# Performance work log

Hardware: AMD Instinct MI355X
Metric: run time of the kernel (lower is better)

Reference implementation:

```python
import jax, jax.numpy as jnp
import numpy as np

NEG_INF = float(np.finfo(np.float32).min)


def setup_inputs() -> dict:
    key = jax.random.key(0)
    k1, k2, k3 = jax.random.split(key, 3)
    n_context, d_model = 4096, 2048
    x = jax.random.normal(k1, (n_context, d_model), dtype=jnp.float32)
    # nn.Linear default init scale ~ 1/sqrt(fan_in); use small weights for numeric sanity
    W_qk = jax.random.normal(k2, (d_model, d_model), dtype=jnp.float32) / np.sqrt(d_model)
    W_ov = jax.random.normal(k3, (d_model, d_model), dtype=jnp.float32) / np.sqrt(d_model)
    return {"x": x, "W_qk": W_qk, "W_ov": W_ov}


def reference(x, W_qk, W_ov):
    # Faithful to: softmax(X @ W_qk.T @ X.T + causal_mask) @ X @ W_ov.T
    # (biases of the torch Linears are never used in forward)
    n = x.shape[0]
    q = x @ W_qk.T                      # [n, d]
    scores = q @ x.T                    # [n, n]  (no 1/sqrt(d) scaling, as in source)
    causal = jnp.tril(jnp.ones((n, n), dtype=bool))
    scores = jnp.where(causal, scores, NEG_INF)  # additive -inf mask equivalent
    attn = jax.nn.softmax(scores, axis=-1)       # [n, n]
    out = (attn @ x) @ W_ov.T                    # [n, d]
    return out
```

## Files before the change

### kernel.cpp

```cpp
#include <hip/hip_runtime.h>
#include <hip/hip_bf16.h>
#include <stdint.h>
#include <stddef.h>

typedef _Float16 f16;
typedef __attribute__((ext_vector_type(8))) _Float16 f16x8;
typedef __attribute__((ext_vector_type(4))) float    f32x4;

constexpr int BM = 128, BN = 128, BK = 64;

#define GLOAD_LDS16(gp, lp)                                        \
    __builtin_amdgcn_global_load_lds(                              \
        (const __attribute__((address_space(1))) unsigned int*)(gp),\
        (__attribute__((address_space(3))) unsigned int*)(lp), 16, 0, 0)


template <int EPI, bool CAUSAL>
__global__ __launch_bounds__(256) void gemm_a2(
    const f16* __restrict__ Ah, const f16* __restrict__ Al,
    const f16* __restrict__ B,
    float* __restrict__ Cf, f16* __restrict__ Co, f16* __restrict__ Clo,
    int M, int N, int K)
{
    const int bx = blockIdx.x;
    const int by = blockIdx.y;
    if (CAUSAL && bx > by) return;

    const int tid   = threadIdx.x;
    const int lane  = tid & 63;
    const int wave  = tid >> 6;
    const int wm    = wave >> 1;
    const int wn    = wave & 1;
    const int lrow  = lane & 15;
    const int lquad = lane >> 4;

    __shared__ f16 sAh[BM * BK];
    __shared__ f16 sAl[BM * BK];
    __shared__ f16 sB [BN * BK];

    const int row0 = by * BM;
    const int col0 = bx * BN;

    const int srow = tid >> 3;
    const int scol = (((tid & 7) ^ ((tid >> 3) & 7))) * 8;
    const int lbase = wave * 512;

    f32x4 acc[4][4];
    const f32x4 fzero = {0.f, 0.f, 0.f, 0.f};
    #pragma unroll
    for (int i = 0; i < 4; ++i)
        #pragma unroll
        for (int j = 0; j < 4; ++j) acc[i][j] = fzero;

    for (int k0 = 0; k0 < K; k0 += BK) {
        __syncthreads();
        #pragma unroll
        for (int r = 0; r < 4; ++r) {
            const int trow = srow + 32 * r;
            const size_t ga = (size_t)(row0 + trow) * K + k0 + scol;
            const size_t gb = (size_t)(col0 + trow) * K + k0 + scol;
            const int ldst = lbase + r * 2048;
            GLOAD_LDS16(&Ah[ga], &sAh[ldst]);
            GLOAD_LDS16(&Al[ga], &sAl[ldst]);
            GLOAD_LDS16(&B [gb], &sB [ldst]);
        }
        __syncthreads();

        #pragma unroll
        for (int kk = 0; kk < 2; ++kk) {
            const int grpA = ((kk * 4 + lquad) ^ (lrow & 7)) * 8;
            f16x8 ah[4], al[4], bv[4];
            #pragma unroll
            for (int mi = 0; mi < 4; ++mi) {
                const int off = (wm * 64 + mi * 16 + lrow) * BK + grpA;
                ah[mi] = *reinterpret_cast<const f16x8*>(&sAh[off]);
                al[mi] = *reinterpret_cast<const f16x8*>(&sAl[off]);
            }
            #pragma unroll
            for (int ni = 0; ni < 4; ++ni)
                bv[ni] = *reinterpret_cast<const f16x8*>(
                    &sB[(wn * 64 + ni * 16 + lrow) * BK + grpA]);

            #pragma unroll
            for (int mi = 0; mi < 4; ++mi)
                #pragma unroll
                for (int ni = 0; ni < 4; ++ni) {
                    acc[mi][ni] = __builtin_amdgcn_mfma_f32_16x16x32_f16(
                        ah[mi], bv[ni], acc[mi][ni], 0, 0, 0);
                    acc[mi][ni] = __builtin_amdgcn_mfma_f32_16x16x32_f16(
                        al[mi], bv[ni], acc[mi][ni], 0, 0, 0);
                }
        }
    }

    #pragma unroll
    for (int mi = 0; mi < 4; ++mi) {
        #pragma unroll
        for (int ni = 0; ni < 4; ++ni) {
            #pragma unroll
            for (int r = 0; r < 4; ++r) {
                const int row = row0 + wm * 64 + mi * 16 + lquad * 4 + r;
                const int col = col0 + wn * 64 + ni * 16 + lrow;
                const size_t idx = (size_t)row * N + col;
                const float v = acc[mi][ni][r];
                if (EPI == 0) {
                    Cf[idx] = v;
                } else {
                    const f16 h = (f16)v;
                    Co[idx]  = h;
                    Clo[idx] = (f16)(v - (float)h);
                }
            }
        }
    }
}

template <int EPI, bool KCAUSAL>
__global__ __launch_bounds__(256) void gemm_plain(
    const f16* __restrict__ A, const f16* __restrict__ B,
    float* __restrict__ Cf, f16* __restrict__ Co,
    int M, int N, int K)
{
    const int bx = blockIdx.x;
    const int by = KCAUSAL ? (gridDim.y - 1 - blockIdx.y) : blockIdx.y;

    const int tid   = threadIdx.x;
    const int lane  = tid & 63;
    const int wave  = tid >> 6;
    const int wm    = wave >> 1;
    const int wn    = wave & 1;
    const int lrow  = lane & 15;
    const int lquad = lane >> 4;

    __shared__ f16 sA[BM * BK];
    __shared__ f16 sB[BN * BK];

    const int row0 = by * BM;
    const int col0 = bx * BN;

    const int srow = tid >> 3;
    const int scol = (((tid & 7) ^ ((tid >> 3) & 7))) * 8;
    const int lbase = wave * 512;

    f32x4 acc[4][4];
    const f32x4 fzero = {0.f, 0.f, 0.f, 0.f};
    #pragma unroll
    for (int i = 0; i < 4; ++i)
        #pragma unroll
        for (int j = 0; j < 4; ++j) acc[i][j] = fzero;

    const int Keff = KCAUSAL ? (by + 1) * BM : K;

    for (int k0 = 0; k0 < Keff; k0 += BK) {
        __syncthreads();
        #pragma unroll
        for (int r = 0; r < 4; ++r) {
            const int trow = srow + 32 * r;
            GLOAD_LDS16(&A[(size_t)(row0 + trow) * K + k0 + scol], &sA[lbase + r * 2048]);
            GLOAD_LDS16(&B[(size_t)(col0 + trow) * K + k0 + scol], &sB[lbase + r * 2048]);
        }
        __syncthreads();

        #pragma unroll
        for (int kk = 0; kk < 2; ++kk) {
            const int grpA = ((kk * 4 + lquad) ^ (lrow & 7)) * 8;
            f16x8 av[4], bv[4];
            #pragma unroll
            for (int mi = 0; mi < 4; ++mi)
                av[mi] = *reinterpret_cast<const f16x8*>(
                    &sA[(wm * 64 + mi * 16 + lrow) * BK + grpA]);
            #pragma unroll
            for (int ni = 0; ni < 4; ++ni)
                bv[ni] = *reinterpret_cast<const f16x8*>(
                    &sB[(wn * 64 + ni * 16 + lrow) * BK + grpA]);

            #pragma unroll
            for (int mi = 0; mi < 4; ++mi)
                #pragma unroll
                for (int ni = 0; ni < 4; ++ni)
                    acc[mi][ni] = __builtin_amdgcn_mfma_f32_16x16x32_f16(
                        av[mi], bv[ni], acc[mi][ni], 0, 0, 0);
        }
    }

    #pragma unroll
    for (int mi = 0; mi < 4; ++mi) {
        #pragma unroll
        for (int ni = 0; ni < 4; ++ni) {
            #pragma unroll
            for (int r = 0; r < 4; ++r) {
                const int row = row0 + wm * 64 + mi * 16 + lquad * 4 + r;
                const int col = col0 + wn * 64 + ni * 16 + lrow;
                const size_t idx = (size_t)row * N + col;
                const float v = acc[mi][ni][r];
                if (EPI == 0) Cf[idx] = v;
                else          Co[idx] = (f16)v;
            }
        }
    }
}

__global__ __launch_bounds__(256) void split_f32_f16(
    const float* __restrict__ in, f16* __restrict__ hi, f16* __restrict__ lo,
    size_t nelem)
{
    const size_t i = ((size_t)blockIdx.x * 256 + threadIdx.x) * 4;
    if (i >= nelem) return;
    const float4 v = *reinterpret_cast<const float4*>(in + i);
    union { f16 h[4]; ushort4 u; } H, L;
    H.h[0] = (f16)v.x; H.h[1] = (f16)v.y; H.h[2] = (f16)v.z; H.h[3] = (f16)v.w;
    *reinterpret_cast<ushort4*>(hi + i) = H.u;
    if (lo) {
        L.h[0] = (f16)(v.x - (float)H.h[0]);
        L.h[1] = (f16)(v.y - (float)H.h[1]);
        L.h[2] = (f16)(v.z - (float)H.h[2]);
        L.h[3] = (f16)(v.w - (float)H.h[3]);
        *reinterpret_cast<ushort4*>(lo + i) = L.u;
    }
}

__global__ __launch_bounds__(256) void softmax_rows(
    const float* __restrict__ S, f16* __restrict__ P, int n)
{
    const int row = blockIdx.x;
    const int len = row + 1;
    const int padlen = ((row >> 7) + 1) << 7;
    const float* srow = S + (size_t)row * n;
    f16* prow = P + (size_t)row * n;
    const int tid = threadIdx.x;
    const int lane = tid & 63, wave = tid >> 6;
    __shared__ float redm[4], reds[4];

    float m = -3.0e38f, s = 0.f;
    for (int j = tid; j < len; j += 256) {
        const float v = srow[j];
        const float mn = fmaxf(m, v);
        s = s * __expf(m - mn) + __expf(v - mn);
        m = mn;
    }
    #pragma unroll
    for (int off = 32; off; off >>= 1) {
        const float mo = __shfl_xor(m, off, 64);
        const float so = __shfl_xor(s, off, 64);
        const float mn = fmaxf(m, mo);
        s = s * __expf(m - mn) + so * __expf(mo - mn);
        m = mn;
    }
    if (lane == 0) { redm[wave] = m; reds[wave] = s; }
    __syncthreads();
    float M = redm[0], Sm = reds[0];
    #pragma unroll
    for (int w = 1; w < 4; ++w) {
        const float mn = fmaxf(M, redm[w]);
        Sm = Sm * __expf(M - mn) + reds[w] * __expf(redm[w] - mn);
        M = mn;
    }
    const float inv = 1.0f / Sm;

    const f16 z = (f16)0.0f;
    for (int j = tid; j < padlen; j += 256)
        prow[j] = (j < len) ? (f16)(__expf(srow[j] - M) * inv) : z;
}

__global__ __launch_bounds__(256) void transpose_f32_f16(
    const float* __restrict__ in, f16* __restrict__ out, int rows, int cols)
{
    __shared__ float tile[32][33];
    const int bx = blockIdx.x;
    const int by = blockIdx.y;
    const int tx = threadIdx.x & 31;
    const int ty = threadIdx.x >> 5;
    #pragma unroll
    for (int r = 0; r < 4; ++r)
        tile[ty + 8 * r][tx] = in[(size_t)(by * 32 + ty + 8 * r) * cols + bx * 32 + tx];
    __syncthreads();
    #pragma unroll
    for (int r = 0; r < 4; ++r)
        out[(size_t)(bx * 32 + ty + 8 * r) * rows + by * 32 + tx] =
            (f16)tile[tx][ty + 8 * r];
}

extern "C" void kernel_launch(void* const* d_in, const int* in_sizes, int n_in,
                              void* d_out, int out_size, void* d_ws, size_t ws_size,
                              hipStream_t stream)
{
    const int n = 4096, d = 2048;
    const float* x   = (const float*)d_in[0];
    const float* Wqk = (const float*)d_in[1];
    const float* Wov = (const float*)d_in[2];
    float* out = (float*)d_out;

    char* ws = (char*)d_ws;
    const size_t MB = 1 << 20;
    f16*   xh   = (f16*)  (ws);
    f16*   xl   = (f16*)  (ws + 16 * MB);
    f16*   Wh   = (f16*)  (ws + 32 * MB);
    f16*   Wovh = (f16*)  (ws + 40 * MB);
    f16*   xTh  = (f16*)  (ws + 48 * MB);
    f16*   qh   = (f16*)  (ws + 64 * MB);
    f16*   ql   = (f16*)  (ws + 80 * MB);
    float* S    = (float*)(ws + 96 * MB);
    f16*   P    = (f16*)  (ws);
    f16*   o    = (f16*)  (ws + 64 * MB);

    const dim3 blk(256);

    split_f32_f16<<<dim3((n * d) / (256 * 4)), blk, 0, stream>>>(x,   xh, xl, (size_t)n * d);
    split_f32_f16<<<dim3((d * d) / (256 * 4)), blk, 0, stream>>>(Wqk, Wh, nullptr, (size_t)d * d);
    split_f32_f16<<<dim3((d * d) / (256 * 4)), blk, 0, stream>>>(Wov, Wovh, nullptr, (size_t)d * d);
    transpose_f32_f16<<<dim3(d / 32, n / 32), blk, 0, stream>>>(x, xTh, n, d);

    gemm_a2<1, false><<<dim3(d / BN, n / BM), blk, 0, stream>>>(
        xh, xl, Wh, nullptr, qh, ql, n, d, d);

    gemm_a2<0, true><<<dim3(n / BN, n / BM), blk, 0, stream>>>(
        qh, ql, xh, S, nullptr, nullptr, n, n, d);

    softmax_rows<<<dim3(n), blk, 0, stream>>>(S, P, n);

    gemm_plain<2, true><<<dim3(d / BN, n / BM), blk, 0, stream>>>(
        P, xTh, nullptr, o, n, d, n);

    gemm_plain<0, false><<<dim3(d / BN, n / BM), blk, 0, stream>>>(
        o, Wovh, out, nullptr, n, d, d);
}
```

Baseline: 446.2 us.

## Use 8-wave 128x256 GEMM kernels with multi-buffered LDS prefetch pipelines

Replaces the two split-precision GEMMs (Q projection and causal scores) with an 8-wave, 128x256-tile kernel that double-buffers LDS and issues the next tile's global-to-LDS loads between MFMA phases. Explicit waitcnt and barriers plus s_setprio keep MFMA issue prioritised. The final output projection moves to a new triple-buffered 8-wave kernel. The aim is to hide global load latency and raise MFMA utilisation. The causal skip becomes coarser (2*bx > by), so some fully masked work is computed, and the larger LDS footprint may limit occupancy.

```diff
diff --git a/kernel.cpp b/kernel.cpp
--- a/kernel.cpp
+++ b/kernel.cpp
@@ -14,9 +14,20 @@
         (const __attribute__((address_space(1))) unsigned int*)(gp),\
         (__attribute__((address_space(3))) unsigned int*)(lp), 16, 0, 0)
 
+#define MFMA_TILE(AV, BV)                                                     \
+    do {                                                                      \
+        __builtin_amdgcn_s_setprio(1);                                        \
+        _Pragma("unroll")                                                     \
+        for (int mi_ = 0; mi_ < 4; ++mi_)                                     \
+            _Pragma("unroll")                                                 \
+            for (int ni_ = 0; ni_ < 4; ++ni_)                                 \
+                acc[mi_][ni_] = __builtin_amdgcn_mfma_f32_16x16x32_f16(       \
+                    (AV)[mi_], (BV)[ni_], acc[mi_][ni_], 0, 0, 0);            \
+        __builtin_amdgcn_s_setprio(0);                                        \
+    } while (0)
 
 template <int EPI, bool CAUSAL>
-__global__ __launch_bounds__(256) void gemm_a2(
+__global__ __launch_bounds__(512, 2) void gemm8_a2(
     const f16* __restrict__ Ah, const f16* __restrict__ Al,
     const f16* __restrict__ B,
     float* __restrict__ Cf, f16* __restrict__ Co, f16* __restrict__ Clo,
@@ -24,74 +35,126 @@
 {
     const int bx = blockIdx.x;
     const int by = blockIdx.y;
-    if (CAUSAL && bx > by) return;
+    if (CAUSAL && 2 * bx > by) return;
 
     const int tid   = threadIdx.x;
     const int lane  = tid & 63;
     const int wave  = tid >> 6;
-    const int wm    = wave >> 1;
-    const int wn    = wave & 1;
+    const int wm    = wave >> 2;
+    const int wn    = wave & 3;
     const int lrow  = lane & 15;
     const int lquad = lane >> 4;
 
-    __shared__ f16 sAh[BM * BK];
-    __shared__ f16 sAl[BM * BK];
-    __shared__ f16 sB [BN * BK];
-
-    const int row0 = by * BM;
-    const int col0 = bx * BN;
+    __shared__ f16 lds[2][32768];
+
+    const int row0 = by * 128;
+    const int col0 = bx * 256;
 
     const int srow = tid >> 3;
-    const int scol = (((tid & 7) ^ ((tid >> 3) & 7))) * 8;
-    const int lbase = wave * 512;
+    const int scol = ((tid & 7) ^ (srow & 7)) * 8;
+    const int loff = wave * 512;
+
+    const int g0 = ((lquad)     ^ (lrow & 7)) * 8;
+    const int g1 = ((4 + lquad) ^ (lrow & 7)) * 8;
+
+    const int arow = (wm * 64 + lrow) * 64;
+    const int brow = (wn * 64 + lrow) * 64 + 16384;
+
+    const f16* gAh = Ah + (size_t)(row0 + srow) * K + scol;
+    const f16* gAl = Al + (size_t)(row0 + srow) * K + scol;
+    const f16* gB  = B  + (size_t)(col0 + srow) * K + scol;
+    const size_t r64 = (size_t)64 * K;
 
     f32x4 acc[4][4];
-    const f32x4 fzero = {0.f, 0.f, 0.f, 0.f};
+    const f32x4 fz = {0.f, 0.f, 0.f, 0.f};
     #pragma unroll
     for (int i = 0; i < 4; ++i)
         #pragma unroll
-        for (int j = 0; j < 4; ++j) acc[i][j] = fzero;
-
-    for (int k0 = 0; k0 < K; k0 += BK) {
-        __syncthreads();
-        #pragma unroll
-        for (int r = 0; r < 4; ++r) {
-            const int trow = srow + 32 * r;
-            const size_t ga = (size_t)(row0 + trow) * K + k0 + scol;
-            const size_t gb = (size_t)(col0 + trow) * K + k0 + scol;
-            const int ldst = lbase + r * 2048;
-            GLOAD_LDS16(&Ah[ga], &sAh[ldst]);
-            GLOAD_LDS16(&Al[ga], &sAl[ldst]);
-            GLOAD_LDS16(&B [gb], &sB [ldst]);
-        }
-        __syncthreads();
-
-        #pragma unroll
-        for (int kk = 0; kk < 2; ++kk) {
-            const int grpA = ((kk * 4 + lquad) ^ (lrow & 7)) * 8;
-            f16x8 ah[4], al[4], bv[4];
-            #pragma unroll
-            for (int mi = 0; mi < 4; ++mi) {
-                const int off = (wm * 64 + mi * 16 + lrow) * BK + grpA;
-                ah[mi] = *reinterpret_cast<const f16x8*>(&sAh[off]);
-                al[mi] = *reinterpret_cast<const f16x8*>(&sAl[off]);
-            }
-            #pragma unroll
-            for (int ni = 0; ni < 4; ++ni)
-                bv[ni] = *reinterpret_cast<const f16x8*>(
-                    &sB[(wn * 64 + ni * 16 + lrow) * BK + grpA]);
-
-            #pragma unroll
-            for (int mi = 0; mi < 4; ++mi)
-                #pragma unroll
-                for (int ni = 0; ni < 4; ++ni) {
-                    acc[mi][ni] = __builtin_amdgcn_mfma_f32_16x16x32_f16(
-                        ah[mi], bv[ni], acc[mi][ni], 0, 0, 0);
-                    acc[mi][ni] = __builtin_amdgcn_mfma_f32_16x16x32_f16(
-                        al[mi], bv[ni], acc[mi][ni], 0, 0, 0);
-                }
-        }
-    }
+        for (int j = 0; j < 4; ++j) acc[i][j] = fz;
+
+    const int nt = K / 64;
+
+    #pragma unroll
+    for (int u = 0; u < 4; ++u)
+        GLOAD_LDS16(gB + u * r64, &lds[0][16384 + u * 4096 + loff]);
+    #pragma unroll
+    for (int u = 0; u < 2; ++u)
+        GLOAD_LDS16(gAh + u * r64, &lds[0][u * 4096 + loff]);
+    #pragma unroll
+    for (int u = 0; u < 2; ++u)
+        GLOAD_LDS16(gAl + u * r64, &lds[0][8192 + u * 4096 + loff]);
+    asm volatile("s_waitcnt vmcnt(2)");
+    __builtin_amdgcn_s_barrier();
+
+    auto tile_body = [&](int t, bool stage) {
+        const int cur = t & 1;
+        const size_t kn = (size_t)(t + 1) * 64;
+        const f16* bufc = &lds[cur][0];
+        f16* bufn = &lds[cur ^ 1][0];
+
+        f16x8 av[4], bv0[4], bv1[4];
+
+        #pragma unroll
+        for (int mi = 0; mi < 4; ++mi)
+            av[mi] = *(const f16x8*)&bufc[arow + mi * 1024 + g0];
+        #pragma unroll
+        for (int ni = 0; ni < 4; ++ni)
+            bv0[ni] = *(const f16x8*)&bufc[brow + ni * 1024 + g0];
+        if (stage) {
+            GLOAD_LDS16(gB + kn,       &bufn[16384 + loff]);
+            GLOAD_LDS16(gB + r64 + kn, &bufn[16384 + 4096 + loff]);
+        }
+        __builtin_amdgcn_s_barrier();
+        asm volatile("s_waitcnt lgkmcnt(0)");
+        MFMA_TILE(av, bv0);
+        __builtin_amdgcn_s_barrier();
+
+        #pragma unroll
+        for (int mi = 0; mi < 4; ++mi)
+            av[mi] = *(const f16x8*)&bufc[arow + mi * 1024 + g1];
+        #pragma unroll
+        for (int ni = 0; ni < 4; ++ni)
+            bv1[ni] = *(const f16x8*)&bufc[brow + ni * 1024 + g1];
+        if (stage) {
+            GLOAD_LDS16(gB + 2 * r64 + kn, &bufn[16384 +  8192 + loff]);
+            GLOAD_LDS16(gB + 3 * r64 + kn, &bufn[16384 + 12288 + loff]);
+            asm volatile("s_waitcnt vmcnt(4)");
+        } else {
+            asm volatile("s_waitcnt vmcnt(0)");
+        }
+        __builtin_amdgcn_s_barrier();
+        asm volatile("s_waitcnt lgkmcnt(0)");
+        MFMA_TILE(av, bv1);
+        __builtin_amdgcn_s_barrier();
+
+        #pragma unroll
+        for (int mi = 0; mi < 4; ++mi)
+            av[mi] = *(const f16x8*)&bufc[8192 + arow + mi * 1024 + g0];
+        if (stage) {
+            GLOAD_LDS16(gAh + kn,       &bufn[loff]);
+            GLOAD_LDS16(gAh + r64 + kn, &bufn[4096 + loff]);
+        }
+        __builtin_amdgcn_s_barrier();
+        asm volatile("s_waitcnt lgkmcnt(0)");
+        MFMA_TILE(av, bv0);
+        __builtin_amdgcn_s_barrier();
+
+        #pragma unroll
+        for (int mi = 0; mi < 4; ++mi)
+            av[mi] = *(const f16x8*)&bufc[8192 + arow + mi * 1024 + g1];
+        if (stage) {
+            GLOAD_LDS16(gAl + kn,       &bufn[ 8192 + loff]);
+            GLOAD_LDS16(gAl + r64 + kn, &bufn[12288 + loff]);
+        }
+        asm volatile("s_waitcnt vmcnt(2)");
+        __builtin_amdgcn_s_barrier();
+        asm volatile("s_waitcnt lgkmcnt(0)");
+        MFMA_TILE(av, bv1);
+        __builtin_amdgcn_s_barrier();
+    };
+
+    for (int t = 0; t < nt - 1; ++t) tile_body(t, true);
+    tile_body(nt - 1, false);
 
     #pragma unroll
     for (int mi = 0; mi < 4; ++mi) {
@@ -115,6 +178,127 @@
     }
 }
 
+template <int EPI>
+__global__ __launch_bounds__(512, 2) void gemm8_1t(
+    const f16* __restrict__ A, const f16* __restrict__ B,
+    float* __restrict__ Cf, f16* __restrict__ Co,
+    int M, int N, int K)
+{
+    const int bx = blockIdx.x;
+    const int by = blockIdx.y;
+
+    const int tid   = threadIdx.x;
+    const int lane  = tid & 63;
+    const int wave  = tid >> 6;
+    const int wm    = wave >> 2;
+    const int wn    = wave & 3;
+    const int lrow  = lane & 15;
+    const int lquad = lane >> 4;
+
+    __shared__ f16 lds[3][24576];
+
+    const int row0 = by * 128;
+    const int col0 = bx * 256;
+
+    const int srow = tid >> 3;
+    const int scol = ((tid & 7) ^ (srow & 7)) * 8;
+    const int loff = wave * 512;
+    const int g0 = ((lquad)     ^ (lrow & 7)) * 8;
+    const int g1 = ((4 + lquad) ^ (lrow & 7)) * 8;
+    const int arow = (wm * 64 + lrow) * 64;
+    const int brow = (wn * 64 + lrow) * 64 + 8192;
+
+    const f16* gA = A + (size_t)(row0 + srow) * K + scol;
+    const f16* gB = B + (size_t)(col0 + srow) * K + scol;
+    const size_t r64 = (size_t)64 * K;
+
+    f32x4 acc[4][4];
+    const f32x4 fz = {0.f, 0.f, 0.f, 0.f};
+    #pragma unroll
+    for (int i = 0; i < 4; ++i)
+        #pragma unroll
+        for (int j = 0; j < 4; ++j) acc[i][j] = fz;
+
+    const int nt = K / 64;
+
+    #pragma unroll
+    for (int tt = 0; tt < 2; ++tt) {
+        const size_t kk = (size_t)tt * 64;
+        #pragma unroll
+        for (int u = 0; u < 4; ++u)
+            GLOAD_LDS16(gB + u * r64 + kk, &lds[tt][8192 + u * 4096 + loff]);
+        #pragma unroll
+        for (int u = 0; u < 2; ++u)
+            GLOAD_LDS16(gA + u * r64 + kk, &lds[tt][u * 4096 + loff]);
+    }
+    asm volatile("s_waitcnt vmcnt(6)");
+    __builtin_amdgcn_s_barrier();
+
+    int cur = 0;
+    for (int t = 0; t < nt; ++t) {
+        const int nb = (cur >= 1) ? (cur - 1) : (cur + 2);
+        const bool stage2 = (t + 2 < nt);
+        const size_t kn = (size_t)(t + 2) * 64;
+        const f16* bufc = &lds[cur][0];
+        f16* bufn = &lds[nb][0];
+
+        f16x8 av[4], bv[4];
+
+        #pragma unroll
+        for (int mi = 0; mi < 4; ++mi)
+            av[mi] = *(const f16x8*)&bufc[arow + mi * 1024 + g0];
+        #pragma unroll
+        for (int ni = 0; ni < 4; ++ni)
+            bv[ni] = *(const f16x8*)&bufc[brow + ni * 1024 + g0];
+        if (stage2) {
+            GLOAD_LDS16(gB + kn,           &bufn[8192 + loff]);
+            GLOAD_LDS16(gB + r64 + kn,     &bufn[8192 + 4096 + loff]);
+            GLOAD_LDS16(gB + 2 * r64 + kn, &bufn[8192 + 8192 + loff]);
+        }
+        __builtin_amdgcn_s_barrier();
+        asm volatile("s_waitcnt lgkmcnt(0)");
+        MFMA_TILE(av, bv);
+        __builtin_amdgcn_s_barrier();
+
+        #pragma unroll
+        for (int mi = 0; mi < 4; ++mi)
+            av[mi] = *(const f16x8*)&bufc[arow + mi * 1024 + g1];
+        #pragma unroll
+        for (int ni = 0; ni < 4; ++ni)
+            bv[ni] = *(const f16x8*)&bufc[brow + ni * 1024 + g1];
+        if (stage2) {
+            GLOAD_LDS16(gB + 3 * r64 + kn, &bufn[8192 + 12288 + loff]);
+            GLOAD_LDS16(gA + kn,           &bufn[loff]);
+            GLOAD_LDS16(gA + r64 + kn,     &bufn[4096 + loff]);
+            asm volatile("s_waitcnt vmcnt(6)");
+        } else {
+            asm volatile("s_waitcnt vmcnt(0)");
+        }
+        __builtin_amdgcn_s_barrier();
+        asm volatile("s_waitcnt lgkmcnt(0)");
+        MFMA_TILE(av, bv);
+        __builtin_amdgcn_s_barrier();
+
+        cur = (cur == 2) ? 0 : cur + 1;
+    }
+
+    #pragma unroll
+    for (int mi = 0; mi < 4; ++mi) {
+        #pragma unroll
+        for (int ni = 0; ni < 4; ++ni) {
+            #pragma unroll
+            for (int r = 0; r < 4; ++r) {
+                const int row = row0 + wm * 64 + mi * 16 + lquad * 4 + r;
+                const int col = col0 + wn * 64 + ni * 16 + lrow;
+                const size_t idx = (size_t)row * N + col;
+                const float v = acc[mi][ni][r];
+                if (EPI == 0) Cf[idx] = v;
+                else          Co[idx] = (f16)v;
+            }
+        }
+    }
+}
+
 template <int EPI, bool KCAUSAL>
 __global__ __launch_bounds__(256) void gemm_plain(
     const f16* __restrict__ A, const f16* __restrict__ B,
@@ -304,16 +488,17 @@
     f16*   o    = (f16*)  (ws + 64 * MB);
 
     const dim3 blk(256);
+    const dim3 blk8(512);
 
     split_f32_f16<<<dim3((n * d) / (256 * 4)), blk, 0, stream>>>(x,   xh, xl, (size_t)n * d);
     split_f32_f16<<<dim3((d * d) / (256 * 4)), blk, 0, stream>>>(Wqk, Wh, nullptr, (size_t)d * d);
     split_f32_f16<<<dim3((d * d) / (256 * 4)), blk, 0, stream>>>(Wov, Wovh, nullptr, (size_t)d * d);
     transpose_f32_f16<<<dim3(d / 32, n / 32), blk, 0, stream>>>(x, xTh, n, d);
 
-    gemm_a2<1, false><<<dim3(d / BN, n / BM), blk, 0, stream>>>(
+    gemm8_a2<1, false><<<dim3(d / 256, n / 128), blk8, 0, stream>>>(
         xh, xl, Wh, nullptr, qh, ql, n, d, d);
 
-    gemm_a2<0, true><<<dim3(n / BN, n / BM), blk, 0, stream>>>(
+    gemm8_a2<0, true><<<dim3(n / 256, n / 128), blk8, 0, stream>>>(
         qh, ql, xh, S, nullptr, nullptr, n, n, d);
 
     softmax_rows<<<dim3(n), blk, 0, stream>>>(S, P, n);
@@ -321,6 +506,6 @@
     gemm_plain<2, true><<<dim3(d / BN, n / BM), blk, 0, stream>>>(
         P, xTh, nullptr, o, n, d, n);
 
-    gemm_plain<0, false><<<dim3(d / BN, n / BM), blk, 0, stream>>>(
+    gemm8_1t<0><<<dim3(d / 256, n / 128), blk8, 0, stream>>>(
         o, Wovh, out, nullptr, n, d, d);
 }
```

Result: faster. 420.1 us (-5.9%).
